# Kernel tuning notes

Measured on AMD Instinct MI355X. Metric: run time of the kernel, lower is better.

## Reference

```python
import jax, jax.numpy as jnp
import numpy as np

K = 3  # kernel_size per dim
DIM = 3
NUM_K = K ** DIM  # 27
# the 2^3 corner offsets of the linear B-spline support
OFFS = np.array([[(s >> d) & 1 for d in range(DIM)] for s in range(2 ** DIM)], dtype=np.int32)  # [8,3]
STRIDES = np.array([K ** d for d in range(DIM)], dtype=np.int32)  # [1,3,9]


def bspline_basis(pseudo):
    """Open B-spline basis, degree 1. pseudo: [E,3] in [0,1]. Returns basis [E,8], kidx [E,8]."""
    v = pseudo * (K - 1)
    i0 = jnp.clip(jnp.floor(v), 0, K - 2)
    f = v - i0  # fractional part in [0,1]
    i0 = i0.astype(jnp.int32)
    offs = jnp.asarray(OFFS)  # [8,3]
    w = jnp.where(offs[None].astype(bool), f[:, None, :], 1.0 - f[:, None, :])  # [E,8,3]
    basis = jnp.prod(w, axis=-1)  # [E,8]
    kidx = jnp.sum((i0[:, None, :] + offs[None]) * jnp.asarray(STRIDES)[None, None, :], axis=-1)  # [E,8]
    return basis, kidx


def spline_conv(x, src, dst, pseudo, W, Wroot, b, num_nodes):
    """SplineConv (degree 1, mean aggregation, root weight + bias)."""
    cout = W.shape[-1]
    xW = jnp.einsum('nc,kco->nko', x, W)  # [N,27,Cout]
    basis, kidx = bspline_basis(pseudo)
    flat = src[:, None] * NUM_K + kidx  # [E,8]
    g = xW.reshape(-1, cout)[flat]  # [E,8,Cout] -- dominant gather
    msg = jnp.einsum('es,eso->eo', basis, g)  # [E,Cout]
    agg = jax.ops.segment_sum(msg, dst, num_segments=num_nodes)
    cnt = jax.ops.segment_sum(jnp.ones((src.shape[0],), x.dtype), dst, num_segments=num_nodes)
    return agg / jnp.maximum(cnt, 1.0)[:, None] + x @ Wroot + b


def seg_max(x, seg, num_segments):
    m = jax.ops.segment_max(x, seg, num_segments=num_segments)
    return jnp.where(jnp.isfinite(m), m, 0.0)  # empty clusters -> 0


def setup_inputs() -> dict:
    key = jax.random.key(0)
    ks = jax.random.split(key, 16)
    N, E, B = 80000, 1280000, 16
    N1, N2 = N // 2, N1 if False else (N // 2) // 2  # N1=40000, N2=20000
    N1 = N // 2
    N2 = N1 // 2
    x = jax.random.normal(ks[0], (N, 2), dtype=jnp.float32)
    edge_index = jax.random.randint(ks[1], (2, E), 0, N, dtype=jnp.int32)
    edge_attr = jax.random.uniform(ks[2], (E, 3), dtype=jnp.float32)
    batch = jnp.sort(jax.random.randint(ks[3], (N,), 0, B, dtype=jnp.int32))
    cluster1 = jax.random.randint(ks[4], (N,), 0, N1, dtype=jnp.int32)
    cluster2 = jax.random.randint(ks[5], (N1,), 0, N2, dtype=jnp.int32)
    W1 = jax.random.normal(ks[6], (NUM_K, 2, 8), dtype=jnp.float32) * 0.3
    root1 = jax.random.normal(ks[7], (2, 8), dtype=jnp.float32) * 0.3
    b1 = jnp.zeros((8,), jnp.float32)
    W2 = jax.random.normal(ks[8], (NUM_K, 8, 16), dtype=jnp.float32) * 0.2
    root2 = jax.random.normal(ks[9], (8, 16), dtype=jnp.float32) * 0.2
    b2 = jnp.zeros((16,), jnp.float32)
    fc1_w = jax.random.normal(ks[10], (16, 64), dtype=jnp.float32) * 0.2
    fc1_b = jnp.zeros((64,), jnp.float32)
    fc2_w = jax.random.normal(ks[11], (64, 1), dtype=jnp.float32) * 0.2
    fc2_b = jnp.zeros((1,), jnp.float32)
    return dict(x=x, edge_index=edge_index, edge_attr=edge_attr, batch=batch,
                cluster1=cluster1, cluster2=cluster2,
                W1=W1, root1=root1, b1=b1, W2=W2, root2=root2, b2=b2,
                fc1_w=fc1_w, fc1_b=fc1_b, fc2_w=fc2_w, fc2_b=fc2_b)


def reference(x, edge_index, edge_attr, batch, cluster1, cluster2,
              W1, root1, b1, W2, root2, b2, fc1_w, fc1_b, fc2_w, fc2_b):
    N = x.shape[0]
    N1 = cluster1.max() * 0 + cluster2.shape[0]  # static: 40000
    N1 = cluster2.shape[0]
    N2 = N1 // 2
    B = 16
    src, dst = edge_index[0], edge_index[1]
    # level 1: SplineConv + ELU
    h = jax.nn.elu(spline_conv(x, src, dst, edge_attr, W1, root1, b1, N))
    # max_pool with precomputed cluster assignment (replaces graclus)
    x1 = seg_max(h, cluster1, N1)
    batch1 = jnp.maximum(jax.ops.segment_max(batch, cluster1, num_segments=N1), 0)
    src2 = cluster1[src]
    dst2 = cluster1[dst]
    # level 2: SplineConv + ELU on coarsened graph
    h2 = jax.nn.elu(spline_conv(x1, src2, dst2, edge_attr, W2, root2, b2, N1))
    x2 = seg_max(h2, cluster2, N2)
    batch2 = jnp.maximum(jax.ops.segment_max(batch1, cluster2, num_segments=N2), 0)
    # scatter_mean over graphs
    s = jax.ops.segment_sum(x2, batch2, num_segments=B)
    c = jax.ops.segment_sum(jnp.ones((N2,), x.dtype), batch2, num_segments=B)
    g = s / jnp.maximum(c, 1.0)[:, None]  # [B,16]
    g = jax.nn.elu(g @ fc1_w + fc1_b)  # dropout is identity in eval mode
    return jax.nn.elu(g @ fc2_w + fc2_b)  # [B,1]
```

## Files before the change

### kernel.cpp

```cpp
#include <hip/hip_runtime.h>
#include <hip/hip_fp16.h>
#include <math.h>


__device__ __forceinline__ float eluf(float x) {
    return x > 0.f ? x : (expf(x) - 1.f);
}

__device__ __forceinline__ float hlo(int v) {
    __half2 h; *(int*)&h = v; return __low2float(h);
}
__device__ __forceinline__ float hhi(int v) {
    __half2 h; *(int*)&h = v; return __high2float(h);
}

typedef _Float16 half2v __attribute__((ext_vector_type(2)));

__device__ __forceinline__ half2v uash2(unsigned u) {
    half2v h; *(unsigned*)&h = u; return h;
}

__device__ __forceinline__ float dot2f(half2v a, half2v b, float c) {
#if __has_builtin(__builtin_amdgcn_fdot2)
    return __builtin_amdgcn_fdot2(a, b, c, false);
#else
    return c + (float)a[0] * (float)b[0] + (float)a[1] * (float)b[1];
#endif
}

#define W1_STRIDE 20
#define W2H_STRIDE 68


__global__ __launch_bounds__(256) void hist_kernel(
    const int* __restrict__ ei, const int* __restrict__ cluster1,
    const int* __restrict__ cluster2,
    int* __restrict__ deg, int* __restrict__ rank,
    int* __restrict__ cdeg, int* __restrict__ rankC,
    int* __restrict__ c2deg, int* __restrict__ rank2,
    int E, int N, int N1)
{
    const int b = (blockIdx.x * 256 + threadIdx.x) * 4;

    if (b + 3 < E && (E & 3) == 0) {
        const int4 d4 = *(const int4*)&ei[E + b];
        int4 r;
        r.x = atomicAdd(&deg[d4.x], 1);
        r.y = atomicAdd(&deg[d4.y], 1);
        r.z = atomicAdd(&deg[d4.z], 1);
        r.w = atomicAdd(&deg[d4.w], 1);
        *(int4*)&rank[b] = r;
    } else {
        for (int j = 0; j < 4; ++j)
            if (b + j < E) rank[b + j] = atomicAdd(&deg[ei[E + b + j]], 1);
    }

    if (b + 3 < N) {
        const int4 c4 = *(const int4*)&cluster1[b];
        int4 r;
        r.x = atomicAdd(&cdeg[c4.x], 1);
        r.y = atomicAdd(&cdeg[c4.y], 1);
        r.z = atomicAdd(&cdeg[c4.z], 1);
        r.w = atomicAdd(&cdeg[c4.w], 1);
        *(int4*)&rankC[b] = r;
    } else {
        for (int j = 0; j < 4; ++j)
            if (b + j < N) rankC[b + j] = atomicAdd(&cdeg[cluster1[b + j]], 1);
    }

    if (b + 3 < N1) {
        const int4 c4 = *(const int4*)&cluster2[b];
        int4 r;
        r.x = atomicAdd(&c2deg[c4.x], 1);
        r.y = atomicAdd(&c2deg[c4.y], 1);
        r.z = atomicAdd(&c2deg[c4.z], 1);
        r.w = atomicAdd(&c2deg[c4.w], 1);
        *(int4*)&rank2[b] = r;
    } else {
        for (int j = 0; j < 4; ++j)
            if (b + j < N1) rank2[b + j] = atomicAdd(&c2deg[cluster2[b + j]], 1);
    }
}

#define SCAN_CHUNK 4096

__global__ __launch_bounds__(256) void scan_a(
    const int* __restrict__ in0, int* __restrict__ out0, int* __restrict__ aux0, int L0, int nb0,
    const int* __restrict__ in1, int* __restrict__ out1, int* __restrict__ aux1, int L1, int nb1,
    const int* __restrict__ in2, int* __restrict__ out2, int* __restrict__ aux2, int L2)
{
    int b = blockIdx.x;
    const int* in; int* out; int* aux; int L;
    if (b < nb0)            { in = in0; out = out0; aux = aux0; L = L0; }
    else if (b < nb0 + nb1) { b -= nb0; in = in1; out = out1; aux = aux1; L = L1; }
    else                    { b -= nb0 + nb1; in = in2; out = out2; aux = aux2; L = L2; }

    __shared__ int ls[256];
    int t = threadIdx.x;
    int base = b * SCAN_CHUNK + t * 16;
    int v[16];
    int s = 0;
#pragma unroll
    for (int j = 0; j < 16; ++j) {
        int val = (base + j < L) ? in[base + j] : 0;
        v[j] = s;
        s += val;
    }
    ls[t] = s;
    __syncthreads();
    for (int off = 1; off < 256; off <<= 1) {
        int tv = (t >= off) ? ls[t - off] : 0;
        __syncthreads();
        ls[t] += tv;
        __syncthreads();
    }
    int excl = ls[t] - s;
#pragma unroll
    for (int j = 0; j < 16; ++j)
        if (base + j < L) out[base + j] = excl + v[j];
    if (t == 255) aux[b] = ls[255];
}

__global__ __launch_bounds__(64) void scan_b(
    int* __restrict__ aux0, int nb0, int* __restrict__ off0, int L0,
    int* __restrict__ aux1, int nb1, int* __restrict__ off1, int L1,
    int* __restrict__ aux2, int nb2, int* __restrict__ off2, int L2)
{
    if (threadIdx.x != 0) return;
    int* aux; int nb; int* off; int L;
    if (blockIdx.x == 0)      { aux = aux0; nb = nb0; off = off0; L = L0; }
    else if (blockIdx.x == 1) { aux = aux1; nb = nb1; off = off1; L = L1; }
    else                      { aux = aux2; nb = nb2; off = off2; L = L2; }
    int run = 0;
    for (int j = 0; j < nb; ++j) { int tv = aux[j]; aux[j] = run; run += tv; }
    off[L] = run;
}

__global__ __launch_bounds__(256) void scan_c(
    int* __restrict__ out0, const int* __restrict__ aux0, int L0, int nb0,
    int* __restrict__ out1, const int* __restrict__ aux1, int L1, int nb1,
    int* __restrict__ out2, const int* __restrict__ aux2, int L2)
{
    int b = blockIdx.x;
    int* out; const int* aux; int L;
    if (b < nb0)            { out = out0; aux = aux0; L = L0; }
    else if (b < nb0 + nb1) { b -= nb0; out = out1; aux = aux1; L = L1; }
    else                    { b -= nb0 + nb1; out = out2; aux = aux2; L = L2; }
    int add = aux[b];
    int base = b * SCAN_CHUNK + threadIdx.x * 16;
#pragma unroll
    for (int j = 0; j < 16; ++j)
        if (base + j < L) out[base + j] += add;
}

__global__ __launch_bounds__(256) void scatB_kernel(
    const int* __restrict__ ei, const float* __restrict__ attr,
    const int* __restrict__ cluster1, const int* __restrict__ cluster2,
    const float2* __restrict__ x, const float* __restrict__ W1,
    const int* __restrict__ doffs, const int* __restrict__ rank,
    const int* __restrict__ coff, const int* __restrict__ rankC,
    const int* __restrict__ c2off, const int* __restrict__ rank2,
    int* __restrict__ nidx, int* __restrict__ n1idx,
    int4* __restrict__ rec4, int E, int N, int N1)
{
    __shared__ float lw[27 * W1_STRIDE];
    for (int i = threadIdx.x; i < 27 * 16; i += 256)
        lw[(i >> 4) * W1_STRIDE + (i & 15)] = W1[i];
    __syncthreads();

    int i = blockIdx.x * 256 + threadIdx.x;
    if (i < E) {
        int s = ei[i], d = ei[E + i];
        int p = doffs[d] + rank[i];

        float vx = attr[3 * i] * 2.f, vy = attr[3 * i + 1] * 2.f, vz = attr[3 * i + 2] * 2.f;
        float ix = fmaxf(fminf(floorf(vx), 1.f), 0.f);
        float iy = fmaxf(fminf(floorf(vy), 1.f), 0.f);
        float iz = fmaxf(fminf(floorf(vz), 1.f), 0.f);
        float fx = vx - ix, fy = vy - iy, fz = vz - iz;
        int ibase = (int)ix + 3 * (int)iy + 9 * (int)iz;

        float2 xv = x[s];
        float wxv[2] = {1.f - fx, fx}, wyv[2] = {1.f - fy, fy}, wzv[2] = {1.f - fz, fz};
        float m[8];
#pragma unroll
        for (int o = 0; o < 8; ++o) m[o] = 0.f;
#pragma unroll
        for (int j = 0; j < 8; ++j) {
            int cx = j & 1, cy = (j >> 1) & 1, cz = j >> 2;
            float w = wxv[cx] * wyv[cy] * wzv[cz];
            const float* Wk = &lw[(ibase + cx + 3 * cy + 9 * cz) * W1_STRIDE];
            float a = w * xv.x, bb = w * xv.y;
            const float4 wa0 = *(const float4*)&Wk[0];
            const float4 wa1 = *(const float4*)&Wk[4];
            const float4 wb0 = *(const float4*)&Wk[8];
            const float4 wb1 = *(const float4*)&Wk[12];
            m[0] += a * wa0.x + bb * wb0.x;
            m[1] += a * wa0.y + bb * wb0.y;
            m[2] += a * wa0.z + bb * wb0.z;
            m[3] += a * wa0.w + bb * wb0.w;
            m[4] += a * wa1.x + bb * wb1.x;
            m[5] += a * wa1.y + bb * wb1.y;
            m[6] += a * wa1.z + bb * wb1.z;
            m[7] += a * wa1.w + bb * wb1.w;
        }

        unsigned hfx = __half_as_ushort(__float2half_rn(fx));
        unsigned hfy = __half_as_ushort(__float2half_rn(fy));
        unsigned hfz = __half_as_ushort(__float2half_rn(fz));
        int s2 = cluster1[s];
        int4 ra = make_int4(s2 | (ibase << 16),
                            (int)(hfx | (hfy << 16)), (int)hfz, 0);
        __half2 h01 = __floats2half2_rn(m[0], m[1]);
        __half2 h23 = __floats2half2_rn(m[2], m[3]);
        __half2 h45 = __floats2half2_rn(m[4], m[5]);
        __half2 h67 = __floats2half2_rn(m[6], m[7]);
        int4 rb = make_int4(*(int*)&h01, *(int*)&h23, *(int*)&h45, *(int*)&h67);
        rec4[2 * (size_t)p]     = ra;
        rec4[2 * (size_t)p + 1] = rb;
    }
    if (i < N)  nidx[coff[cluster1[i]] + rankC[i]] = i;
    if (i < N1) n1idx[c2off[cluster2[i]] + rank2[i]] = i;
}

__global__ __launch_bounds__(256) void reduce1_kernel(
    const int* __restrict__ doffs, const unsigned short* __restrict__ recU,
    float* __restrict__ M1, int N)
{
    int t = blockIdx.x * 256 + threadIdx.x;
    if (t >= N * 8) return;
    int d = t >> 3, ch = t & 7;
    int beg = doffs[d], end = doffs[d + 1];
    float acc = 0.f;
    for (int p = beg; p < end; ++p)
        acc += __half2float(__ushort_as_half(recU[(size_t)p * 16 + 8 + ch]));
    M1[t] = acc / fmaxf((float)(end - beg), 1.f);
}

__global__ __launch_bounds__(256) void node1_kernel(
    const int* __restrict__ coff, const int* __restrict__ nidx,
    const float* __restrict__ M1, const float2* __restrict__ x,
    const float* __restrict__ root1, const float* __restrict__ b1,
    const int* __restrict__ batch,
    float* __restrict__ x1c, unsigned short* __restrict__ x1chU,
    int* __restrict__ batch1, int N1)
{
    int t = blockIdx.x * 256 + threadIdx.x;
    if (t >= N1 * 8) return;
    int c = t >> 3, ch = t & 7;
    int cb = coff[c], ce = coff[c + 1];
    float r0 = root1[ch], r1 = root1[8 + ch], bo = b1[ch];
    float hm = -INFINITY;
    int bm = 0;
    for (int idx = cb; idx < ce; ++idx) {
        int d = nidx[idx];
        float2 xv = x[d];
        float h = eluf(M1[d * 8 + ch] + xv.x * r0 + xv.y * r1 + bo);
        hm = fmaxf(hm, h);
        bm = max(bm, batch[d]);
    }
    if (ce == cb) hm = 0.f;
    x1c[t] = hm;
    x1chU[t] = __half_as_ushort(__float2half_rn(hm));
    if (ch == 0) batch1[c] = bm;
}

__global__ __launch_bounds__(256) void edge2m_kernel(
    const int4* __restrict__ rec4, const unsigned short* __restrict__ x1chU,
    const float* __restrict__ W2, unsigned short* __restrict__ msg2h, int E)
{
    __shared__ unsigned lwh[27 * W2H_STRIDE];
    for (int i = threadIdx.x; i < 27 * 64; i += 256) {
        int k = i >> 6, r = i & 63;
        int o = r >> 2, c2 = r & 3;
        float a = W2[(k * 8 + 2 * c2) * 16 + o];
        float b = W2[(k * 8 + 2 * c2 + 1) * 16 + o];
        __half2 h = __floats2half2_rn(a, b);
        lwh[k * W2H_STRIDE + r] = *(unsigned*)&h;
    }
    __syncthreads();

    int t = blockIdx.x * 256 + threadIdx.x;
    if (t >= E * 4) return;
    int p = t >> 2, oq = t & 3;
    int4 m = rec4[2 * (size_t)p];
    int s2 = m.x & 0xFFFF;
    int ibase = (m.x >> 16) & 31;
    float fx = hlo(m.y), fy = hhi(m.y), fz = hlo(m.z);

    const uint4 xv4 = *(const uint4*)&x1chU[(size_t)s2 * 8];
    half2v xh0 = uash2(xv4.x), xh1 = uash2(xv4.y),
           xh2 = uash2(xv4.z), xh3 = uash2(xv4.w);

    float wx0 = 1.f - fx, wy0 = 1.f - fy, wz0 = 1.f - fz;
    float acc0 = 0.f, acc1 = 0.f, acc2 = 0.f, acc3 = 0.f;
#pragma unroll
    for (int j = 0; j < 8; ++j) {
        int cx = j & 1, cy = (j >> 1) & 1, cz = j >> 2;
        float w = (cx ? fx : wx0) * (cy ? fy : wy0) * (cz ? fz : wz0);
        int k = ibase + cx + 3 * cy + 9 * cz;
        const unsigned* base = &lwh[k * W2H_STRIDE + oq * 16];
        uint4 v0 = *(const uint4*)(base);
        uint4 v1 = *(const uint4*)(base + 4);
        uint4 v2 = *(const uint4*)(base + 8);
        uint4 v3 = *(const uint4*)(base + 12);
        float s0 = dot2f(xh0, uash2(v0.x), dot2f(xh1, uash2(v0.y),
                   dot2f(xh2, uash2(v0.z), dot2f(xh3, uash2(v0.w), 0.f))));
        float s1 = dot2f(xh0, uash2(v1.x), dot2f(xh1, uash2(v1.y),
                   dot2f(xh2, uash2(v1.z), dot2f(xh3, uash2(v1.w), 0.f))));
        float s2v = dot2f(xh0, uash2(v2.x), dot2f(xh1, uash2(v2.y),
                    dot2f(xh2, uash2(v2.z), dot2f(xh3, uash2(v2.w), 0.f))));
        float s3 = dot2f(xh0, uash2(v3.x), dot2f(xh1, uash2(v3.y),
                   dot2f(xh2, uash2(v3.z), dot2f(xh3, uash2(v3.w), 0.f))));
        acc0 = fmaf(w, s0, acc0);
        acc1 = fmaf(w, s1, acc1);
        acc2 = fmaf(w, s2v, acc2);
        acc3 = fmaf(w, s3, acc3);
    }
    __half2 lo = __floats2half2_rn(acc0, acc1);
    __half2 hi = __floats2half2_rn(acc2, acc3);
    uint2 outv = make_uint2(*(unsigned*)&lo, *(unsigned*)&hi);
    *(uint2*)&msg2h[(size_t)p * 16 + oq * 4] = outv;
}

__global__ __launch_bounds__(256) void reduce2_kernel(
    const int* __restrict__ coff, const int* __restrict__ nidx,
    const int* __restrict__ doffs, const unsigned short* __restrict__ msg2h,
    float* __restrict__ M2, int N1)
{
    int t = blockIdx.x * 256 + threadIdx.x;
    if (t >= N1 * 16) return;
    int c = t >> 4, o = t & 15;
    float acc = 0.f;
    int cnt = 0;
    int cb = coff[c], ce = coff[c + 1];
    for (int idx = cb; idx < ce; ++idx) {
        int d = nidx[idx];
        int beg = doffs[d], end = doffs[d + 1];
        cnt += end - beg;
        for (int p = beg; p < end; ++p)
            acc += __half2float(__ushort_as_half(msg2h[(size_t)p * 16 + o]));
    }
    M2[t] = acc / fmaxf((float)cnt, 1.f);
}

__global__ __launch_bounds__(256) void node2_kernel(
    const int* __restrict__ c2off, const int* __restrict__ n1idx,
    const float* __restrict__ M2, const float* __restrict__ x1c,
    const float* __restrict__ root2, const float* __restrict__ b2,
    const int* __restrict__ batch1,
    float* __restrict__ gsum, float* __restrict__ gcnt, int N2)
{
    __shared__ float ls[16 * 16];
    __shared__ float lc[16];
    for (int i = threadIdx.x; i < 256; i += 256) ls[i] = 0.f;
    if (threadIdx.x < 16) lc[threadIdx.x] = 0.f;
    __syncthreads();

    int c2 = blockIdx.x * 256 + threadIdx.x;
    if (c2 < N2) {
        int cb = c2off[c2], ce = c2off[c2 + 1];
        float hm[16];
#pragma unroll
        for (int o = 0; o < 16; ++o) hm[o] = -INFINITY;
        int bm = 0;
        for (int idx = cb; idx < ce; ++idx) {
            int n1 = n1idx[idx];
            const float4* xr4 = (const float4*)&x1c[(size_t)n1 * 8];
            float4 xa = xr4[0], xb = xr4[1];
            float xr[8] = {xa.x, xa.y, xa.z, xa.w, xb.x, xb.y, xb.z, xb.w};
#pragma unroll
            for (int o = 0; o < 16; ++o) {
                float v = M2[(size_t)n1 * 16 + o] + b2[o];
#pragma unroll
                for (int c8 = 0; c8 < 8; ++c8) v += xr[c8] * root2[c8 * 16 + o];
                hm[o] = fmaxf(hm[o], eluf(v));
            }
            bm = max(bm, batch1[n1]);
        }
        if (ce == cb) {
#pragma unroll
            for (int o = 0; o < 16; ++o) hm[o] = 0.f;
        }
#pragma unroll
        for (int o = 0; o < 16; ++o) atomicAdd(&ls[bm * 16 + o], hm[o]);
        atomicAdd(&lc[bm], 1.f);
    }
    __syncthreads();
    for (int i = threadIdx.x; i < 256; i += 256) unsafeAtomicAdd(&gsum[i], ls[i]);
    if (threadIdx.x < 16) unsafeAtomicAdd(&gcnt[threadIdx.x], lc[threadIdx.x]);
}

__global__ __launch_bounds__(256) void head_kernel(
    const float* __restrict__ gsum, const float* __restrict__ gcnt,
    const float* __restrict__ fc1_w, const float* __restrict__ fc1_b,
    const float* __restrict__ fc2_w, const float* __restrict__ fc2_b,
    float* __restrict__ out, int B)
{
    __shared__ float g[16 * 16];
    __shared__ float h1[16 * 64];
    int t = threadIdx.x;
    if (t < B * 16) {
        int b = t >> 4;
        g[t] = gsum[t] / fmaxf(gcnt[b], 1.f);
    }
    __syncthreads();
    for (int j = t; j < B * 64; j += 256) {
        int b = j >> 6, jj = j & 63;
        float s = fc1_b[jj];
#pragma unroll
        for (int c = 0; c < 16; ++c) s += g[b * 16 + c] * fc1_w[c * 64 + jj];
        h1[j] = eluf(s);
    }
    __syncthreads();
    if (t < B) {
        float s = fc2_b[0];
#pragma unroll
        for (int j = 0; j < 64; ++j) s += h1[t * 64 + j] * fc2_w[j];
        out[t] = eluf(s);
    }
}

extern "C" void kernel_launch(void* const* d_in, const int* in_sizes, int n_in,
                              void* d_out, int out_size, void* d_ws, size_t ws_size,
                              hipStream_t stream)
{
    const float* x        = (const float*)d_in[0];
    const int*   ei       = (const int*)  d_in[1];
    const float* attr     = (const float*)d_in[2];
    const int*   batch    = (const int*)  d_in[3];
    const int*   cluster1 = (const int*)  d_in[4];
    const int*   cluster2 = (const int*)  d_in[5];
    const float* W1       = (const float*)d_in[6];
    const float* root1    = (const float*)d_in[7];
    const float* b1       = (const float*)d_in[8];
    const float* W2       = (const float*)d_in[9];
    const float* root2    = (const float*)d_in[10];
    const float* b2       = (const float*)d_in[11];
    const float* fc1_w    = (const float*)d_in[12];
    const float* fc1_b    = (const float*)d_in[13];
    const float* fc2_w    = (const float*)d_in[14];
    const float* fc2_b    = (const float*)d_in[15];

    const int N  = in_sizes[0] / 2;
    const int E  = in_sizes[1] / 2;
    const int N1 = in_sizes[5];
    const int N2 = N1 / 2;
    const int B  = out_size;

    const int nb0 = (N  + SCAN_CHUNK - 1) / SCAN_CHUNK;
    const int nb1 = (N1 + SCAN_CHUNK - 1) / SCAN_CHUNK;
    const int nb2 = (N2 + SCAN_CHUNK - 1) / SCAN_CHUNK;

    int* wi = (int*)d_ws;
    size_t off = 0;
    auto alloc = [&](size_t n, size_t align = 1) {
        off = (off + align - 1) & ~(align - 1);
        size_t r = off; off += n; return r;
    };
    int*   deg    = wi + alloc(N);
    int*   cdeg   = wi + alloc(N1);
    int*   c2deg  = wi + alloc(N2);
    float* gsum   = (float*)(wi + alloc((size_t)B * 16));
    float* gcnt   = (float*)(wi + alloc(B));
    const size_t zcount = off;
    int*   doffs  = wi + alloc(N + 1);
    int*   coff   = wi + alloc(N1 + 1);
    int*   c2off  = wi + alloc(N2 + 1);
    int*   auxA   = wi + alloc(nb0);
    int*   auxB   = wi + alloc(nb1);
    int*   auxC   = wi + alloc(nb2);
    int*   rank   = wi + alloc(E);
    int*   rankC  = wi + alloc(N);
    int*   rank2  = wi + alloc(N1);
    int*   nidx   = wi + alloc(N);
    int*   n1idx  = wi + alloc(N1);
    int4*  rec4   = (int4*)(wi + alloc((size_t)E * 8, 8));
    unsigned short* msg2h = (unsigned short*)(wi + alloc((size_t)E * 8, 4));
    float* M1     = (float*)(wi + alloc((size_t)N * 8, 4));
    float* x1c    = (float*)(wi + alloc((size_t)N1 * 8, 4));
    unsigned short* x1chU = (unsigned short*)(wi + alloc((size_t)N1 * 4, 4));
    int*   batch1 = wi + alloc(N1);
    float* M2     = (float*)(wi + alloc((size_t)N1 * 16, 4));
    (void)ws_size;

    hipMemsetAsync(d_ws, 0, zcount * sizeof(int), stream);

    const int eb = (E + 255) / 256;
    int maxL = E > N ? E : N;
    if (N1 > maxL) maxL = N1;
    hist_kernel<<<(maxL + 1023) / 1024, 256, 0, stream>>>(
        ei, cluster1, cluster2, deg, rank, cdeg, rankC, c2deg, rank2, E, N, N1);
    scan_a<<<nb0 + nb1 + nb2, 256, 0, stream>>>(deg, doffs, auxA, N, nb0,
                                                cdeg, coff, auxB, N1, nb1,
                                                c2deg, c2off, auxC, N2);
    scan_b<<<3, 64, 0, stream>>>(auxA, nb0, doffs, N,
                                 auxB, nb1, coff, N1,
                                 auxC, nb2, c2off, N2);
    scan_c<<<nb0 + nb1 + nb2, 256, 0, stream>>>(doffs, auxA, N, nb0,
                                                coff, auxB, N1, nb1,
                                                c2off, auxC, N2);
    scatB_kernel<<<eb, 256, 0, stream>>>(ei, attr, cluster1, cluster2,
                                         (const float2*)x, W1,
                                         doffs, rank, coff, rankC, c2off, rank2,
                                         nidx, n1idx, rec4, E, N, N1);
    reduce1_kernel<<<(N * 8 + 255) / 256, 256, 0, stream>>>(
        doffs, (const unsigned short*)rec4, M1, N);
    node1_kernel<<<(N1 * 8 + 255) / 256, 256, 0, stream>>>(
        coff, nidx, M1, (const float2*)x, root1, b1, batch,
        x1c, x1chU, batch1, N1);
    edge2m_kernel<<<(E * 4 + 255) / 256, 256, 0, stream>>>(
        rec4, x1chU, W2, msg2h, E);
    reduce2_kernel<<<(N1 * 16 + 255) / 256, 256, 0, stream>>>(
        coff, nidx, doffs, msg2h, M2, N1);
    node2_kernel<<<(N2 + 255) / 256, 256, 0, stream>>>(
        c2off, n1idx, M2, x1c, root2, b2, batch1, gsum, gcnt, N2);
    head_kernel<<<1, 256, 0, stream>>>(gsum, gcnt, fc1_w, fc1_b, fc2_w, fc2_b,
                                       (float*)d_out, B);
}
```

Before: 367.4 us.

## Fuse per-edge level-2 message compute into cluster-owned reduction; fuse reduce1 into node1

Merges reduce1 into node1, so the per-node mean over the level-1 records is computed inside the cluster max loop and the M1 buffer goes away. Merges edge2m into reduce2: each thread, owning one cluster and one output channel, recomputes the B-spline-weighted W2 dot product for every incoming edge and accumulates directly. This removes the msg2h intermediate (E×16 halves) write and read, plus two launches. The cost is that each edge's record and source features are now read by all 16 per-channel threads, and load imbalance across clusters with many edges can serialize work.

```diff
diff --git a/kernel.cpp b/kernel.cpp
--- a/kernel.cpp
+++ b/kernel.cpp
@@ -29,7 +29,7 @@
 }
 
 #define W1_STRIDE 20
-#define W2H_STRIDE 68
+#define W2R_STRIDE 108
 
 
 __global__ __launch_bounds__(256) void hist_kernel(
@@ -223,23 +223,10 @@
     if (i < N1) n1idx[c2off[cluster2[i]] + rank2[i]] = i;
 }
 
-__global__ __launch_bounds__(256) void reduce1_kernel(
+__global__ __launch_bounds__(256) void node1R_kernel(
+    const int* __restrict__ coff, const int* __restrict__ nidx,
     const int* __restrict__ doffs, const unsigned short* __restrict__ recU,
-    float* __restrict__ M1, int N)
-{
-    int t = blockIdx.x * 256 + threadIdx.x;
-    if (t >= N * 8) return;
-    int d = t >> 3, ch = t & 7;
-    int beg = doffs[d], end = doffs[d + 1];
-    float acc = 0.f;
-    for (int p = beg; p < end; ++p)
-        acc += __half2float(__ushort_as_half(recU[(size_t)p * 16 + 8 + ch]));
-    M1[t] = acc / fmaxf((float)(end - beg), 1.f);
-}
-
-__global__ __launch_bounds__(256) void node1_kernel(
-    const int* __restrict__ coff, const int* __restrict__ nidx,
-    const float* __restrict__ M1, const float2* __restrict__ x,
+    const float2* __restrict__ x,
     const float* __restrict__ root1, const float* __restrict__ b1,
     const int* __restrict__ batch,
     float* __restrict__ x1c, unsigned short* __restrict__ x1chU,
@@ -254,8 +241,13 @@
     int bm = 0;
     for (int idx = cb; idx < ce; ++idx) {
         int d = nidx[idx];
+        int beg = doffs[d], end = doffs[d + 1];
+        float acc = 0.f;
+        for (int p = beg; p < end; ++p)
+            acc += __half2float(__ushort_as_half(recU[(size_t)p * 16 + 8 + ch]));
+        float m1 = acc / fmaxf((float)(end - beg), 1.f);
         float2 xv = x[d];
-        float h = eluf(M1[d * 8 + ch] + xv.x * r0 + xv.y * r1 + bo);
+        float h = eluf(m1 + xv.x * r0 + xv.y * r1 + bo);
         hm = fmaxf(hm, h);
         bm = max(bm, batch[d]);
     }
@@ -265,83 +257,57 @@
     if (ch == 0) batch1[c] = bm;
 }
 
-__global__ __launch_bounds__(256) void edge2m_kernel(
-    const int4* __restrict__ rec4, const unsigned short* __restrict__ x1chU,
-    const float* __restrict__ W2, unsigned short* __restrict__ msg2h, int E)
-{
-    __shared__ unsigned lwh[27 * W2H_STRIDE];
-    for (int i = threadIdx.x; i < 27 * 64; i += 256) {
-        int k = i >> 6, r = i & 63;
-        int o = r >> 2, c2 = r & 3;
+__global__ __launch_bounds__(256) void edge2r_kernel(
+    const int* __restrict__ coff, const int* __restrict__ nidx,
+    const int* __restrict__ doffs, const int4* __restrict__ rec4,
+    const unsigned short* __restrict__ x1chU, const float* __restrict__ W2,
+    float* __restrict__ M2, int N1)
+{
+    __shared__ unsigned lwh[16 * W2R_STRIDE];
+    for (int j = threadIdx.x; j < 16 * 108; j += 256) {
+        int o = j / 108, rem = j - o * 108;
+        int k = rem >> 2, c2 = rem & 3;
         float a = W2[(k * 8 + 2 * c2) * 16 + o];
         float b = W2[(k * 8 + 2 * c2 + 1) * 16 + o];
         __half2 h = __floats2half2_rn(a, b);
-        lwh[k * W2H_STRIDE + r] = *(unsigned*)&h;
-    }
-    __syncthreads();
-
-    int t = blockIdx.x * 256 + threadIdx.x;
-    if (t >= E * 4) return;
-    int p = t >> 2, oq = t & 3;
-    int4 m = rec4[2 * (size_t)p];
-    int s2 = m.x & 0xFFFF;
-    int ibase = (m.x >> 16) & 31;
-    float fx = hlo(m.y), fy = hhi(m.y), fz = hlo(m.z);
-
-    const uint4 xv4 = *(const uint4*)&x1chU[(size_t)s2 * 8];
-    half2v xh0 = uash2(xv4.x), xh1 = uash2(xv4.y),
-           xh2 = uash2(xv4.z), xh3 = uash2(xv4.w);
-
-    float wx0 = 1.f - fx, wy0 = 1.f - fy, wz0 = 1.f - fz;
-    float acc0 = 0.f, acc1 = 0.f, acc2 = 0.f, acc3 = 0.f;
-#pragma unroll
-    for (int j = 0; j < 8; ++j) {
-        int cx = j & 1, cy = (j >> 1) & 1, cz = j >> 2;
-        float w = (cx ? fx : wx0) * (cy ? fy : wy0) * (cz ? fz : wz0);
-        int k = ibase + cx + 3 * cy + 9 * cz;
-        const unsigned* base = &lwh[k * W2H_STRIDE + oq * 16];
-        uint4 v0 = *(const uint4*)(base);
-        uint4 v1 = *(const uint4*)(base + 4);
-        uint4 v2 = *(const uint4*)(base + 8);
-        uint4 v3 = *(const uint4*)(base + 12);
-        float s0 = dot2f(xh0, uash2(v0.x), dot2f(xh1, uash2(v0.y),
-                   dot2f(xh2, uash2(v0.z), dot2f(xh3, uash2(v0.w), 0.f))));
-        float s1 = dot2f(xh0, uash2(v1.x), dot2f(xh1, uash2(v1.y),
-                   dot2f(xh2, uash2(v1.z), dot2f(xh3, uash2(v1.w), 0.f))));
-        float s2v = dot2f(xh0, uash2(v2.x), dot2f(xh1, uash2(v2.y),
-                    dot2f(xh2, uash2(v2.z), dot2f(xh3, uash2(v2.w), 0.f))));
-        float s3 = dot2f(xh0, uash2(v3.x), dot2f(xh1, uash2(v3.y),
-                   dot2f(xh2, uash2(v3.z), dot2f(xh3, uash2(v3.w), 0.f))));
-        acc0 = fmaf(w, s0, acc0);
-        acc1 = fmaf(w, s1, acc1);
-        acc2 = fmaf(w, s2v, acc2);
-        acc3 = fmaf(w, s3, acc3);
-    }
-    __half2 lo = __floats2half2_rn(acc0, acc1);
-    __half2 hi = __floats2half2_rn(acc2, acc3);
-    uint2 outv = make_uint2(*(unsigned*)&lo, *(unsigned*)&hi);
-    *(uint2*)&msg2h[(size_t)p * 16 + oq * 4] = outv;
-}
-
-__global__ __launch_bounds__(256) void reduce2_kernel(
-    const int* __restrict__ coff, const int* __restrict__ nidx,
-    const int* __restrict__ doffs, const unsigned short* __restrict__ msg2h,
-    float* __restrict__ M2, int N1)
-{
+        lwh[j] = *(unsigned*)&h;
+    }
+    __syncthreads();
+
     int t = blockIdx.x * 256 + threadIdx.x;
     if (t >= N1 * 16) return;
     int c = t >> 4, o = t & 15;
-    float acc = 0.f;
+    const unsigned* wrow = &lwh[o * W2R_STRIDE];
+    float accA = 0.f, accB = 0.f;
     int cnt = 0;
     int cb = coff[c], ce = coff[c + 1];
     for (int idx = cb; idx < ce; ++idx) {
         int d = nidx[idx];
         int beg = doffs[d], end = doffs[d + 1];
         cnt += end - beg;
-        for (int p = beg; p < end; ++p)
-            acc += __half2float(__ushort_as_half(msg2h[(size_t)p * 16 + o]));
-    }
-    M2[t] = acc / fmaxf((float)cnt, 1.f);
+        for (int p = beg; p < end; ++p) {
+            int4 m = rec4[2 * (size_t)p];
+            int s2 = m.x & 0xFFFF;
+            int ibase = (m.x >> 16) & 31;
+            float fx = hlo(m.y), fy = hhi(m.y), fz = hlo(m.z);
+            const uint4 xv4 = *(const uint4*)&x1chU[(size_t)s2 * 8];
+            half2v xh0 = uash2(xv4.x), xh1 = uash2(xv4.y),
+                   xh2 = uash2(xv4.z), xh3 = uash2(xv4.w);
+            float wx0 = 1.f - fx, wy0 = 1.f - fy, wz0 = 1.f - fz;
+#pragma unroll
+            for (int j = 0; j < 8; ++j) {
+                int cx = j & 1, cy = (j >> 1) & 1, cz = j >> 2;
+                float w = (cx ? fx : wx0) * (cy ? fy : wy0) * (cz ? fz : wz0);
+                int k = ibase + cx + 3 * cy + 9 * cz;
+                uint4 wv = *(const uint4*)&wrow[k * 4];
+                float s = dot2f(xh0, uash2(wv.x), dot2f(xh1, uash2(wv.y),
+                          dot2f(xh2, uash2(wv.z), dot2f(xh3, uash2(wv.w), 0.f))));
+                if (j & 1) accB = fmaf(w, s, accB);
+                else       accA = fmaf(w, s, accA);
+            }
+        }
+    }
+    M2[t] = (accA + accB) / fmaxf((float)cnt, 1.f);
 }
 
 __global__ __launch_bounds__(256) void node2_kernel(
@@ -476,8 +442,6 @@
     int*   nidx   = wi + alloc(N);
     int*   n1idx  = wi + alloc(N1);
     int4*  rec4   = (int4*)(wi + alloc((size_t)E * 8, 8));
-    unsigned short* msg2h = (unsigned short*)(wi + alloc((size_t)E * 8, 4));
-    float* M1     = (float*)(wi + alloc((size_t)N * 8, 4));
     float* x1c    = (float*)(wi + alloc((size_t)N1 * 8, 4));
     unsigned short* x1chU = (unsigned short*)(wi + alloc((size_t)N1 * 4, 4));
     int*   batch1 = wi + alloc(N1);
@@ -504,15 +468,11 @@
                                          (const float2*)x, W1,
                                          doffs, rank, coff, rankC, c2off, rank2,
                                          nidx, n1idx, rec4, E, N, N1);
-    reduce1_kernel<<<(N * 8 + 255) / 256, 256, 0, stream>>>(
-        doffs, (const unsigned short*)rec4, M1, N);
-    node1_kernel<<<(N1 * 8 + 255) / 256, 256, 0, stream>>>(
-        coff, nidx, M1, (const float2*)x, root1, b1, batch,
-        x1c, x1chU, batch1, N1);
-    edge2m_kernel<<<(E * 4 + 255) / 256, 256, 0, stream>>>(
-        rec4, x1chU, W2, msg2h, E);
-    reduce2_kernel<<<(N1 * 16 + 255) / 256, 256, 0, stream>>>(
-        coff, nidx, doffs, msg2h, M2, N1);
+    node1R_kernel<<<(N1 * 8 + 255) / 256, 256, 0, stream>>>(
+        coff, nidx, doffs, (const unsigned short*)rec4, (const float2*)x,
+        root1, b1, batch, x1c, x1chU, batch1, N1);
+    edge2r_kernel<<<(N1 * 16 + 255) / 256, 256, 0, stream>>>(
+        coff, nidx, doffs, rec4, x1chU, W2, M2, N1);
     node2_kernel<<<(N2 + 255) / 256, 256, 0, stream>>>(
         c2off, n1idx, M2, x1c, root2, b2, batch1, gsum, gcnt, N2);
     head_kernel<<<1, 256, 0, stream>>>(gsum, gcnt, fc1_w, fc1_b, fc2_w, fc2_b,
```

Result: slower. 416.2 us (+13.3%).
